# Performance work log

Hardware: AMD Instinct MI355X
Metric: run time of the kernel (lower is better)

## Reference

```python
import jax, jax.numpy as jnp
import numpy as np

B, N, D = 4, 2048, 512
H, DA, DL = 8, 64, 64  # heads, attention_dim, linear_dim
EPS = 1e-6


def _layer_norm(x, eps=EPS):
    # F.layer_norm with no affine params
    mu = jnp.mean(x, axis=-1, keepdims=True)
    var = jnp.var(x, axis=-1, keepdims=True)
    return (x - mu) * jax.lax.rsqrt(var + eps)


def setup_inputs() -> dict:
    key = jax.random.key(0)
    k1, k2, k3, k4 = jax.random.split(key, 4)
    x = jax.random.normal(k1, (B, N, D), dtype=jnp.float32)
    # causal (lower-triangular) valid-attention mask, float {0,1}, shape (B,1,N,N)
    attention_mask = jnp.broadcast_to(
        jnp.tril(jnp.ones((N, N), dtype=jnp.float32))[None, None], (B, 1, N, N)
    )
    # _uvqk: (D, 2*H*DL + 2*H*DA), init normal(0, 0.02)
    uvqk = 0.02 * jax.random.normal(k2, (D, 2 * H * DL + 2 * H * DA), dtype=jnp.float32)
    # _o: Linear(H*DL -> D), xavier uniform
    fan_in, fan_out = H * DL, D
    limit = float(np.sqrt(6.0 / (fan_in + fan_out)))
    o_weight = jax.random.uniform(k3, (fan_out, fan_in), dtype=jnp.float32, minval=-limit, maxval=limit)
    o_bias = jnp.zeros((D,), dtype=jnp.float32)
    return {"x": x, "attention_mask": attention_mask, "uvqk": uvqk,
            "o_weight": o_weight, "o_bias": o_bias}


def reference(x, attention_mask, uvqk, o_weight, o_bias):
    b, n, _ = x.shape
    normed_x = _layer_norm(x)
    mm = jax.nn.silu(normed_x @ uvqk)  # fused uvqk projection + silu
    u, v, q, k = jnp.split(mm, [H * DL, 2 * H * DL, 2 * H * DL + H * DA], axis=-1)
    qh = q.reshape(b, n, H, DA)
    kh = k.reshape(b, n, H, DA)
    vh = v.reshape(b, n, H, DL)
    # silu-activated (non-softmax) attention with mask
    qk = jnp.einsum('bnhd,bmhd->bhnm', qh, kh)
    qk = jax.nn.silu(qk) / n
    qk = qk * attention_mask  # (B,1,N,N) broadcast over heads
    attn = jnp.einsum('bhnm,bmhd->bnhd', qk, vh).reshape(b, n, H * DL)
    # gated norm + output proj + residual
    o_input = u * _layer_norm(attn)
    return o_input @ o_weight.T + o_bias + x
```

## Files before the change

kernel.cpp:

```cpp
#include <hip/hip_runtime.h>

typedef __bf16 bf16x8 __attribute__((ext_vector_type(8)));
typedef float f32x4 __attribute__((ext_vector_type(4)));
typedef float f32x16 __attribute__((ext_vector_type(16)));

__device__ __forceinline__ unsigned short f2bf(float f) {
  return __builtin_bit_cast(unsigned short, (__bf16)f);
}
__device__ __forceinline__ float bfu2f(unsigned short b) {
  unsigned int u = ((unsigned int)b) << 16;
  return __builtin_bit_cast(float, u);
}
__device__ __forceinline__ float silu_f(float x) {
  return x * __builtin_amdgcn_rcpf(1.0f + __expf(-x));
}
__device__ __forceinline__ unsigned pk2(float a, float b) {
  return (unsigned)f2bf(a) | ((unsigned)f2bf(b) << 16);
}

template<int CPR, int NI, bool SWZ = false>
__device__ __forceinline__ void stage16(const __bf16* __restrict__ g, int ld,
                                        __bf16* lds, int wave, int lane) {
#pragma unroll
  for (int t = 0; t < NI; ++t) {
    int cb = (wave * NI + t) * 64;
    int c = cb + lane;
    int row = c / CPR;
    int colb = c % CPR;
    if (SWZ) colb ^= (row & 3);
    __builtin_amdgcn_global_load_lds(
        (const __attribute__((address_space(1))) unsigned int*)(g + row * ld + colb * 8),
        (__attribute__((address_space(3))) unsigned int*)(lds + cb * 8),
        16, 0, 0);
  }
}


__global__ void k_tr_uvqk(const float* __restrict__ uvqk, __bf16* __restrict__ uvqkT) {
  __shared__ float tile[32][33];
  int n0 = blockIdx.x * 32, k0 = blockIdx.y * 32;
  int tx = threadIdx.x, ty = threadIdx.y;
  for (int i = ty; i < 32; i += 8)
    tile[i][tx] = uvqk[(k0 + i) * 2048 + n0 + tx];
  __syncthreads();
  for (int i = ty; i < 32; i += 8)
    uvqkT[(n0 + i) * 512 + k0 + tx] = (__bf16)tile[tx][i];
}

__global__ void k_prep(const float* __restrict__ x, __bf16* __restrict__ nx,
                       const float* __restrict__ ow, __bf16* __restrict__ owb) {
  int bid = blockIdx.x, t = threadIdx.x;
  if (bid >= 8192) {
    int i = (bid - 8192) * 128 + t;
    float4 v = ((const float4*)ow)[i];
    ushort4 o4;
    o4.x = f2bf(v.x); o4.y = f2bf(v.y); o4.z = f2bf(v.z); o4.w = f2bf(v.w);
    ((ushort4*)owb)[i] = o4;
    return;
  }
  float4 v = ((const float4*)(x + (size_t)bid * 512))[t];
  float s = v.x + v.y + v.z + v.w;
  float ss = v.x * v.x + v.y * v.y + v.z * v.z + v.w * v.w;
#pragma unroll
  for (int o = 32; o > 0; o >>= 1) { s += __shfl_down(s, o); ss += __shfl_down(ss, o); }
  __shared__ float red[4];
  if ((t & 63) == 0) { red[(t >> 6) * 2] = s; red[(t >> 6) * 2 + 1] = ss; }
  __syncthreads();
  s = red[0] + red[2]; ss = red[1] + red[3];
  float mu = s * (1.0f / 512.0f);
  float var = ss * (1.0f / 512.0f) - mu * mu;
  float rs = rsqrtf(var + 1e-6f);
  ushort4 o4;
  o4.x = f2bf((v.x - mu) * rs); o4.y = f2bf((v.y - mu) * rs);
  o4.z = f2bf((v.z - mu) * rs); o4.w = f2bf((v.w - mu) * rs);
  ((ushort4*)(nx + (size_t)bid * 512))[t] = o4;
}

__global__ __launch_bounds__(256, 2) void k_proj(
    const __bf16* __restrict__ A, const __bf16* __restrict__ Bt,
    __bf16* __restrict__ u, __bf16* __restrict__ qn,
    __bf16* __restrict__ kn, __bf16* __restrict__ vt) {
  __shared__ __bf16 As[128 * 32], Bs[128 * 32];
  int tid = threadIdx.x, wave = tid >> 6, lane = tid & 63;
  int lr = lane & 15, lq = lane >> 4;
  int bn = blockIdx.x, bm = blockIdx.y;
  const __bf16* Ag = A + (size_t)bm * 128 * 512;
  const __bf16* Bg = Bt + (size_t)bn * 128 * 512;
  int wm = (wave >> 1) * 64, wn = (wave & 1) * 64;
  f32x4 acc[4][4] = {};
  for (int k0 = 0; k0 < 512; k0 += 32) {
    stage16<4, 2>(Ag + k0, 512, As, wave, lane);
    stage16<4, 2>(Bg + k0, 512, Bs, wave, lane);
    __syncthreads();
    bf16x8 a[4], bb[4];
#pragma unroll
    for (int i = 0; i < 4; ++i)
      a[i] = *(const bf16x8*)(As + (wm + i * 16 + lr) * 32 + lq * 8);
#pragma unroll
    for (int j = 0; j < 4; ++j)
      bb[j] = *(const bf16x8*)(Bs + (wn + j * 16 + lr) * 32 + lq * 8);
#pragma unroll
    for (int i = 0; i < 4; ++i)
#pragma unroll
      for (int j = 0; j < 4; ++j)
        acc[i][j] = __builtin_amdgcn_mfma_f32_16x16x32_bf16(a[i], bb[j], acc[i][j], 0, 0, 0);
    __syncthreads();
  }
  int seg = bn >> 2;
  int cb = (bn & 3) * 128 + wn;
  int rb0 = bm * 128 + wm + lq * 4;
  if (seg == 1) {
    const float sc = 1.0f / 2048.0f;
#pragma unroll
    for (int i = 0; i < 4; ++i) {
      int rb = rb0 + i * 16;
      int b = rb >> 11, n = rb & 2047;
#pragma unroll
      for (int j = 0; j < 4; ++j) {
        int c = cb + j * 16 + lr;
        ushort4 w;
        w.x = f2bf(silu_f(acc[i][j][0]) * sc);
        w.y = f2bf(silu_f(acc[i][j][1]) * sc);
        w.z = f2bf(silu_f(acc[i][j][2]) * sc);
        w.w = f2bf(silu_f(acc[i][j][3]) * sc);
        *(ushort4*)(vt + ((size_t)(b * 512 + c)) * 2048 + n) = w;
      }
    }
  } else {
    __bf16* dst = (seg == 0) ? u : ((seg == 2) ? qn : kn);
#pragma unroll
    for (int i = 0; i < 4; ++i) {
      int rb = rb0 + i * 16;
#pragma unroll
      for (int j = 0; j < 4; ++j) {
        int c = cb + j * 16 + lr;
#pragma unroll
        for (int rg = 0; rg < 4; ++rg)
          dst[(size_t)(rb + rg) * 512 + c] = (__bf16)silu_f(acc[i][j][rg]);
      }
    }
  }
}

__global__ __launch_bounds__(256, 2) void k_attn(
    const __bf16* __restrict__ qn, const __bf16* __restrict__ kn,
    const __bf16* __restrict__ vt, __bf16* __restrict__ attn) {
  __shared__ __bf16 lds[40960];
  __bf16* Qs = lds;
  __bf16* Ks0 = lds + 8192;
  __bf16* Ks1 = lds + 16384;
  __bf16* Vs0 = lds + 24576;
  __bf16* Vs1 = lds + 32768;

  int bh = blockIdx.x;
  int yy = blockIdx.y;
  int qt = (yy < 8) ? yy : 23 - yy;
  int b = bh >> 3, h = bh & 7;
  int tid = threadIdx.x, wave = tid >> 6, lane = tid & 63;
  int l31 = lane & 31, lh = lane >> 5;
  int n0 = qt * 128;
  const __bf16* Qg = qn + (size_t)(b * 2048 + n0) * 512 + h * 64;
  const __bf16* Kg = kn + (size_t)(b * 2048) * 512 + h * 64;
  const __bf16* Vg = vt + (size_t)(b * 512 + h * 64) * 2048;

  stage16<4, 2, true>(Qg, 512, Qs, wave, lane);
  stage16<4, 2, true>(Qg + 32, 512, Qs + 4096, wave, lane);
  stage16<4, 2, true>(Kg, 512, Ks0, wave, lane);
  stage16<4, 2, true>(Kg + 32, 512, Ks0 + 4096, wave, lane);
#pragma unroll
  for (int p = 0; p < 4; ++p)
    stage16<4, 1, true>(Vg + p * 32, 2048, Vs0 + p * 2048, wave, lane);
  __syncthreads();

  int wm = (wave >> 1) * 64, wn = (wave & 1) * 64;

  bf16x8 qf[2][4];
#pragma unroll
  for (int j = 0; j < 2; ++j)
#pragma unroll
    for (int ks = 0; ks < 4; ++ks) {
      int row = wn + j * 32 + l31;
      int kidx = ks * 16 + lh * 8;
      qf[j][ks] = *(const bf16x8*)(Qs + (kidx >> 5) * 4096 + row * 32 +
                                   (((kidx & 31)) ^ ((row & 3) * 8)));
    }

  f32x16 po[2][2] = {};

  for (int mt = 0; mt <= qt; ++mt) {
    const __bf16* Kc = (mt & 1) ? Ks1 : Ks0;
    const __bf16* Vc = (mt & 1) ? Vs1 : Vs0;
    if (mt < qt) {
      __bf16* Kn_ = (mt & 1) ? Ks0 : Ks1;
      __bf16* Vn_ = (mt & 1) ? Vs0 : Vs1;
      const __bf16* Kgm = Kg + (size_t)(mt + 1) * 128 * 512;
      stage16<4, 2, true>(Kgm, 512, Kn_, wave, lane);
      stage16<4, 2, true>(Kgm + 32, 512, Kn_ + 4096, wave, lane);
#pragma unroll
      for (int p = 0; p < 4; ++p)
        stage16<4, 1, true>(Vg + (mt + 1) * 128 + p * 32, 2048, Vn_ + p * 2048, wave, lane);
    }
    f32x16 s[2][2] = {};
#pragma unroll
    for (int ks = 0; ks < 4; ++ks) {
      int kidx = ks * 16 + lh * 8;
      bf16x8 ak[2];
#pragma unroll
      for (int i = 0; i < 2; ++i) {
        int row = wm + i * 32 + l31;
        ak[i] = *(const bf16x8*)(Kc + (kidx >> 5) * 4096 + row * 32 +
                                 ((kidx & 31) ^ ((row & 3) * 8)));
      }
#pragma unroll
      for (int i = 0; i < 2; ++i)
#pragma unroll
        for (int j = 0; j < 2; ++j)
          s[i][j] = __builtin_amdgcn_mfma_f32_32x32x16_bf16(ak[i], qf[j][ks], s[i][j], 0, 0, 0);
    }
    bool diag = (mt == qt);
    bool lo = (lh == 0);
    bf16x8 pf[2][4];
#pragma unroll
    for (int i = 0; i < 2; ++i) {
      int mbase = wm + i * 32;
#pragma unroll
      for (int j = 0; j < 2; ++j) {
        int nbase = wn + j * 32;
        bool full = diag && (mbase > nbase + 31);
        unsigned pk[8];
        if (full) {
#pragma unroll
          for (int q = 0; q < 8; ++q) pk[q] = 0u;
        } else {
          bool dtile = diag && (mbase + 31 > nbase);
          int mb = mbase + 4 * lh;
          int ncol = nbase + l31;
          float vv[16];
#pragma unroll
          for (int r = 0; r < 16; ++r) {
            float xx = s[i][j][r];
            float p = xx * __builtin_amdgcn_rcpf(1.0f + __expf(-xx));
            if (dtile) {
              int row = mb + (r & 3) + 8 * (r >> 2);
              if (row > ncol) p = 0.0f;
            }
            vv[r] = p;
          }
#pragma unroll
          for (int q = 0; q < 8; ++q) pk[q] = pk2(vv[2 * q], vv[2 * q + 1]);
        }
        unsigned xa = __shfl_xor(lo ? pk[2] : pk[0], 32);
        unsigned xb = __shfl_xor(lo ? pk[3] : pk[1], 32);
        unsigned xc = __shfl_xor(lo ? pk[6] : pk[4], 32);
        unsigned xd = __shfl_xor(lo ? pk[7] : pk[5], 32);
        union { bf16x8 v; unsigned u[4]; } f0, f1;
        f0.u[0] = lo ? pk[0] : xa;  f0.u[1] = lo ? pk[1] : xb;
        f0.u[2] = lo ? xa : pk[2];  f0.u[3] = lo ? xb : pk[3];
        f1.u[0] = lo ? pk[4] : xc;  f1.u[1] = lo ? pk[5] : xd;
        f1.u[2] = lo ? xc : pk[6];  f1.u[3] = lo ? xd : pk[7];
        pf[j][i * 2 + 0] = f0.v;
        pf[j][i * 2 + 1] = f1.v;
      }
    }
#pragma unroll
    for (int t4 = 0; t4 < 4; ++t4) {
      int kidx = wm + t4 * 16 + lh * 8;
      bf16x8 av[2];
#pragma unroll
      for (int idl = 0; idl < 2; ++idl) {
        int row = idl * 32 + l31;
        av[idl] = *(const bf16x8*)(Vc + (kidx >> 5) * 2048 + row * 32 +
                                   ((kidx & 31) ^ ((row & 3) * 8)));
      }
#pragma unroll
      for (int idl = 0; idl < 2; ++idl)
#pragma unroll
        for (int j = 0; j < 2; ++j)
          po[idl][j] = __builtin_amdgcn_mfma_f32_32x32x16_bf16(av[idl], pf[j][t4], po[idl][j], 0, 0, 0);
    }
    __syncthreads();
  }

  float* red = (float*)lds;
  if (wave >= 2) {
    float* dst = red + (wave - 2) * 4096;
#pragma unroll
    for (int idl = 0; idl < 2; ++idl)
#pragma unroll
      for (int j = 0; j < 2; ++j)
#pragma unroll
        for (int r = 0; r < 16; ++r)
          dst[((idl * 2 + j) * 16 + r) * 64 + lane] = po[idl][j][r];
  }
  __syncthreads();
  __bf16* bo = lds + 24576;
  if (wave < 2) {
    float* src = red + wave * 4096;
#pragma unroll
    for (int idl = 0; idl < 2; ++idl)
#pragma unroll
      for (int j = 0; j < 2; ++j) {
#pragma unroll
        for (int r = 0; r < 16; ++r)
          po[idl][j][r] += src[((idl * 2 + j) * 16 + r) * 64 + lane];
        int nrow = wn + j * 32 + l31;
#pragma unroll
        for (int g = 0; g < 4; ++g) {
          int dl0 = idl * 32 + g * 8 + lh * 4;
          ushort4 w;
          w.x = f2bf(po[idl][j][4 * g + 0]); w.y = f2bf(po[idl][j][4 * g + 1]);
          w.z = f2bf(po[idl][j][4 * g + 2]); w.w = f2bf(po[idl][j][4 * g + 3]);
          *(ushort4*)(bo + nrow * 72 + dl0) = w;
        }
      }
  }
  __syncthreads();
  {
    int n = tid >> 1, part = tid & 1;
    __bf16* gdst = attn + (size_t)(b * 2048 + n0 + n) * 512 + h * 64 + part * 32;
    const __bf16* lsrc = bo + n * 72 + part * 32;
#pragma unroll
    for (int c = 0; c < 4; ++c)
      *(uint4*)(gdst + c * 8) = *(const uint4*)(lsrc + c * 8);
  }
}

__global__ void k_oinput(const __bf16* __restrict__ attn, const __bf16* __restrict__ u,
                         __bf16* __restrict__ oin) {
  int r = blockIdx.x, t = threadIdx.x;
  ushort4 a4 = ((const ushort4*)(attn + (size_t)r * 512))[t];
  float a0 = bfu2f(a4.x), a1 = bfu2f(a4.y), a2 = bfu2f(a4.z), a3 = bfu2f(a4.w);
  float s = a0 + a1 + a2 + a3;
  float ss = a0 * a0 + a1 * a1 + a2 * a2 + a3 * a3;
#pragma unroll
  for (int o = 32; o > 0; o >>= 1) { s += __shfl_down(s, o); ss += __shfl_down(ss, o); }
  __shared__ float red[4];
  if ((t & 63) == 0) { red[(t >> 6) * 2] = s; red[(t >> 6) * 2 + 1] = ss; }
  __syncthreads();
  s = red[0] + red[2]; ss = red[1] + red[3];
  float mu = s * (1.0f / 512.0f);
  float var = ss * (1.0f / 512.0f) - mu * mu;
  float rs = rsqrtf(var + 1e-6f);
  ushort4 u4 = ((const ushort4*)(u + (size_t)r * 512))[t];
  ushort4 o4;
  o4.x = f2bf(bfu2f(u4.x) * (a0 - mu) * rs);
  o4.y = f2bf(bfu2f(u4.y) * (a1 - mu) * rs);
  o4.z = f2bf(bfu2f(u4.z) * (a2 - mu) * rs);
  o4.w = f2bf(bfu2f(u4.w) * (a3 - mu) * rs);
  ((ushort4*)(oin + (size_t)r * 512))[t] = o4;
}

__global__ __launch_bounds__(256, 2) void k_out(
    const __bf16* __restrict__ A, const __bf16* __restrict__ Bt,
    const float* __restrict__ bias, const float* __restrict__ x,
    float* __restrict__ out) {
  __shared__ __bf16 As[128 * 32], Bs[128 * 32];
  int tid = threadIdx.x, wave = tid >> 6, lane = tid & 63;
  int lr = lane & 15, lq = lane >> 4;
  int bn = blockIdx.x, bm = blockIdx.y;
  const __bf16* Ag = A + (size_t)bm * 128 * 512;
  const __bf16* Bg = Bt + (size_t)bn * 128 * 512;
  int wm = (wave >> 1) * 64, wn = (wave & 1) * 64;
  f32x4 acc[4][4] = {};
  for (int k0 = 0; k0 < 512; k0 += 32) {
    stage16<4, 2>(Ag + k0, 512, As, wave, lane);
    stage16<4, 2>(Bg + k0, 512, Bs, wave, lane);
    __syncthreads();
    bf16x8 a[4], bb[4];
#pragma unroll
    for (int i = 0; i < 4; ++i)
      a[i] = *(const bf16x8*)(As + (wm + i * 16 + lr) * 32 + lq * 8);
#pragma unroll
    for (int j = 0; j < 4; ++j)
      bb[j] = *(const bf16x8*)(Bs + (wn + j * 16 + lr) * 32 + lq * 8);
#pragma unroll
    for (int i = 0; i < 4; ++i)
#pragma unroll
      for (int j = 0; j < 4; ++j)
        acc[i][j] = __builtin_amdgcn_mfma_f32_16x16x32_bf16(a[i], bb[j], acc[i][j], 0, 0, 0);
    __syncthreads();
  }
  int cb = bn * 128 + wn;
  int rb0 = bm * 128 + wm + lq * 4;
#pragma unroll
  for (int j = 0; j < 4; ++j) {
    int c = cb + j * 16 + lr;
    float bv = bias[c];
#pragma unroll
    for (int i = 0; i < 4; ++i) {
      int rb = rb0 + i * 16;
#pragma unroll
      for (int rg = 0; rg < 4; ++rg) {
        size_t idx = (size_t)(rb + rg) * 512 + c;
        out[idx] = acc[i][j][rg] + bv + x[idx];
      }
    }
  }
}

extern "C" void kernel_launch(void* const* d_in, const int* in_sizes, int n_in,
                              void* d_out, int out_size, void* d_ws, size_t ws_size,
                              hipStream_t stream) {
  const float* x = (const float*)d_in[0];
  const float* uvqk = (const float*)d_in[2];
  const float* ow = (const float*)d_in[3];
  const float* ob = (const float*)d_in[4];
  float* out = (float*)d_out;

  char* w = (char*)d_ws;
  const size_t MB8 = 8u * 1024 * 1024;
  __bf16* nx    = (__bf16*)(w);
  __bf16* u     = (__bf16*)(w + MB8);
  __bf16* qn    = (__bf16*)(w + 2 * MB8);
  __bf16* kn    = (__bf16*)(w + 3 * MB8);
  __bf16* vt    = (__bf16*)(w + 4 * MB8);
  __bf16* uvqkT = (__bf16*)(w + 5 * MB8);
  __bf16* owb   = (__bf16*)(w + 5 * MB8 + 2097152);
  __bf16* attn  = nx;
  __bf16* o_in  = qn;

  k_tr_uvqk<<<dim3(64, 16), dim3(32, 8), 0, stream>>>(uvqk, uvqkT);
  k_prep<<<8704, 128, 0, stream>>>(x, nx, ow, owb);
  k_proj<<<dim3(16, 64), 256, 0, stream>>>(nx, uvqkT, u, qn, kn, vt);
  k_attn<<<dim3(32, 16), 256, 0, stream>>>(qn, kn, vt, attn);
  k_oinput<<<8192, 128, 0, stream>>>(attn, u, o_in);
  k_out<<<dim3(4, 64), 256, 0, stream>>>(o_in, owb, ob, x, out);
}
```

Baseline: 223.2 us.

## Pair causal query tiles per attention block, halve query tile, widen GEMM K-step

The attention kernel now has each block handle 64 query rows and process two paired query tiles (p and 15-p) in sequence, which evens out causal work per block. The grid becomes 32x8x2. K and V tiles are staged with a single XOR-swizzled 64- or 128-wide layout instead of split 32-wide sub-tiles. The projection and output GEMMs now stage 64-wide K slices with an XOR swizzle, halving the barrier count, and their launch bounds are raised to 3 blocks per CU. The cost is that every attention block re-streams K/V for both query tiles, and per-block MFMA work is smaller.

```diff
diff --git a/kernel.cpp b/kernel.cpp
--- a/kernel.cpp
+++ b/kernel.cpp
@@ -18,7 +18,7 @@
   return (unsigned)f2bf(a) | ((unsigned)f2bf(b) << 16);
 }
 
-template<int CPR, int NI, bool SWZ = false>
+template<int CPR, int NI, int SWZ>
 __device__ __forceinline__ void stage16(const __bf16* __restrict__ g, int ld,
                                         __bf16* lds, int wave, int lane) {
 #pragma unroll
@@ -26,8 +26,7 @@
     int cb = (wave * NI + t) * 64;
     int c = cb + lane;
     int row = c / CPR;
-    int colb = c % CPR;
-    if (SWZ) colb ^= (row & 3);
+    int colb = (c % CPR) ^ (row & SWZ);
     __builtin_amdgcn_global_load_lds(
         (const __attribute__((address_space(1))) unsigned int*)(g + row * ld + colb * 8),
         (__attribute__((address_space(3))) unsigned int*)(lds + cb * 8),
@@ -76,11 +75,11 @@
   ((ushort4*)(nx + (size_t)bid * 512))[t] = o4;
 }
 
-__global__ __launch_bounds__(256, 2) void k_proj(
+__global__ __launch_bounds__(256, 3) void k_proj(
     const __bf16* __restrict__ A, const __bf16* __restrict__ Bt,
     __bf16* __restrict__ u, __bf16* __restrict__ qn,
     __bf16* __restrict__ kn, __bf16* __restrict__ vt) {
-  __shared__ __bf16 As[128 * 32], Bs[128 * 32];
+  __shared__ __bf16 As[128 * 64], Bs[128 * 64];
   int tid = threadIdx.x, wave = tid >> 6, lane = tid & 63;
   int lr = lane & 15, lq = lane >> 4;
   int bn = blockIdx.x, bm = blockIdx.y;
@@ -88,29 +87,36 @@
   const __bf16* Bg = Bt + (size_t)bn * 128 * 512;
   int wm = (wave >> 1) * 64, wn = (wave & 1) * 64;
   f32x4 acc[4][4] = {};
-  for (int k0 = 0; k0 < 512; k0 += 32) {
-    stage16<4, 2>(Ag + k0, 512, As, wave, lane);
-    stage16<4, 2>(Bg + k0, 512, Bs, wave, lane);
-    __syncthreads();
-    bf16x8 a[4], bb[4];
-#pragma unroll
-    for (int i = 0; i < 4; ++i)
-      a[i] = *(const bf16x8*)(As + (wm + i * 16 + lr) * 32 + lq * 8);
-#pragma unroll
-    for (int j = 0; j < 4; ++j)
-      bb[j] = *(const bf16x8*)(Bs + (wn + j * 16 + lr) * 32 + lq * 8);
-#pragma unroll
-    for (int i = 0; i < 4; ++i)
-#pragma unroll
-      for (int j = 0; j < 4; ++j)
-        acc[i][j] = __builtin_amdgcn_mfma_f32_16x16x32_bf16(a[i], bb[j], acc[i][j], 0, 0, 0);
+  for (int k0 = 0; k0 < 512; k0 += 64) {
+    stage16<8, 4, 7>(Ag + k0, 512, As, wave, lane);
+    stage16<8, 4, 7>(Bg + k0, 512, Bs, wave, lane);
+    __syncthreads();
+#pragma unroll
+    for (int kk = 0; kk < 2; ++kk) {
+      int b = kk * 4 + lq;
+      bf16x8 a[4], bb[4];
+#pragma unroll
+      for (int i = 0; i < 4; ++i) {
+        int row = wm + i * 16 + lr;
+        a[i] = *(const bf16x8*)(As + row * 64 + ((b ^ (row & 7)) * 8));
+      }
+#pragma unroll
+      for (int j = 0; j < 4; ++j) {
+        int row = wn + j * 16 + lr;
+        bb[j] = *(const bf16x8*)(Bs + row * 64 + ((b ^ (row & 7)) * 8));
+      }
+#pragma unroll
+      for (int i = 0; i < 4; ++i)
+#pragma unroll
+        for (int j = 0; j < 4; ++j)
+          acc[i][j] = __builtin_amdgcn_mfma_f32_16x16x32_bf16(a[i], bb[j], acc[i][j], 0, 0, 0);
+    }
     __syncthreads();
   }
   int seg = bn >> 2;
   int cb = (bn & 3) * 128 + wn;
   int rb0 = bm * 128 + wm + lq * 4;
   if (seg == 1) {
-    const float sc = 1.0f / 2048.0f;
 #pragma unroll
     for (int i = 0; i < 4; ++i) {
       int rb = rb0 + i * 16;
@@ -119,10 +125,10 @@
       for (int j = 0; j < 4; ++j) {
         int c = cb + j * 16 + lr;
         ushort4 w;
-        w.x = f2bf(silu_f(acc[i][j][0]) * sc);
-        w.y = f2bf(silu_f(acc[i][j][1]) * sc);
-        w.z = f2bf(silu_f(acc[i][j][2]) * sc);
-        w.w = f2bf(silu_f(acc[i][j][3]) * sc);
+        w.x = f2bf(silu_f(acc[i][j][0]) * (1.0f / 2048.0f));
+        w.y = f2bf(silu_f(acc[i][j][1]) * (1.0f / 2048.0f));
+        w.z = f2bf(silu_f(acc[i][j][2]) * (1.0f / 2048.0f));
+        w.w = f2bf(silu_f(acc[i][j][3]) * (1.0f / 2048.0f));
         *(ushort4*)(vt + ((size_t)(b * 512 + c)) * 2048 + n) = w;
       }
     }
@@ -145,106 +151,92 @@
 __global__ __launch_bounds__(256, 2) void k_attn(
     const __bf16* __restrict__ qn, const __bf16* __restrict__ kn,
     const __bf16* __restrict__ vt, __bf16* __restrict__ attn) {
-  __shared__ __bf16 lds[40960];
-  __bf16* Qs = lds;
-  __bf16* Ks0 = lds + 8192;
-  __bf16* Ks1 = lds + 16384;
-  __bf16* Vs0 = lds + 24576;
-  __bf16* Vs1 = lds + 32768;
+  __shared__ __bf16 lds[36864];
+  __bf16* Qs  = lds;
+  __bf16* Ks0 = lds + 4096;
+  __bf16* Ks1 = lds + 12288;
+  __bf16* Vs0 = lds + 20480;
+  __bf16* Vs1 = lds + 28672;
 
   int bh = blockIdx.x;
-  int yy = blockIdx.y;
-  int qt = (yy < 8) ? yy : 23 - yy;
-  int b = bh >> 3, h = bh & 7;
+  int p = blockIdx.y;
+  int half = blockIdx.z;
+  int b = bh >> 3, hd = bh & 7;
   int tid = threadIdx.x, wave = tid >> 6, lane = tid & 63;
   int l31 = lane & 31, lh = lane >> 5;
-  int n0 = qt * 128;
-  const __bf16* Qg = qn + (size_t)(b * 2048 + n0) * 512 + h * 64;
-  const __bf16* Kg = kn + (size_t)(b * 2048) * 512 + h * 64;
-  const __bf16* Vg = vt + (size_t)(b * 512 + h * 64) * 2048;
-
-  stage16<4, 2, true>(Qg, 512, Qs, wave, lane);
-  stage16<4, 2, true>(Qg + 32, 512, Qs + 4096, wave, lane);
-  stage16<4, 2, true>(Kg, 512, Ks0, wave, lane);
-  stage16<4, 2, true>(Kg + 32, 512, Ks0 + 4096, wave, lane);
-#pragma unroll
-  for (int p = 0; p < 4; ++p)
-    stage16<4, 1, true>(Vg + p * 32, 2048, Vs0 + p * 2048, wave, lane);
-  __syncthreads();
-
-  int wm = (wave >> 1) * 64, wn = (wave & 1) * 64;
-
-  bf16x8 qf[2][4];
-#pragma unroll
-  for (int j = 0; j < 2; ++j)
+  int wm = (wave >> 1) * 64, wn = (wave & 1) * 32;
+  const __bf16* Kg = kn + (size_t)(b * 2048) * 512 + hd * 64;
+  const __bf16* Vg = vt + (size_t)(b * 512 + hd * 64) * 2048;
+
+  for (int ph = 0; ph < 2; ++ph) {
+    int qtx = ph ? (15 - p) : p;
+    int n0 = qtx * 128;
+    const __bf16* Qg = qn + (size_t)(b * 2048 + n0 + half * 64) * 512 + hd * 64;
+    if (ph) __syncthreads();
+    stage16<8, 2, 7>(Qg, 512, Qs, wave, lane);
+    stage16<8, 4, 7>(Kg, 512, Ks0, wave, lane);
+    stage16<16, 4, 15>(Vg, 2048, Vs0, wave, lane);
+    __syncthreads();
+
+    bf16x8 qf[4];
 #pragma unroll
     for (int ks = 0; ks < 4; ++ks) {
-      int row = wn + j * 32 + l31;
-      int kidx = ks * 16 + lh * 8;
-      qf[j][ks] = *(const bf16x8*)(Qs + (kidx >> 5) * 4096 + row * 32 +
-                                   (((kidx & 31)) ^ ((row & 3) * 8)));
-    }
-
-  f32x16 po[2][2] = {};
-
-  for (int mt = 0; mt <= qt; ++mt) {
-    const __bf16* Kc = (mt & 1) ? Ks1 : Ks0;
-    const __bf16* Vc = (mt & 1) ? Vs1 : Vs0;
-    if (mt < qt) {
-      __bf16* Kn_ = (mt & 1) ? Ks0 : Ks1;
-      __bf16* Vn_ = (mt & 1) ? Vs0 : Vs1;
-      const __bf16* Kgm = Kg + (size_t)(mt + 1) * 128 * 512;
-      stage16<4, 2, true>(Kgm, 512, Kn_, wave, lane);
-      stage16<4, 2, true>(Kgm + 32, 512, Kn_ + 4096, wave, lane);
-#pragma unroll
-      for (int p = 0; p < 4; ++p)
-        stage16<4, 1, true>(Vg + (mt + 1) * 128 + p * 32, 2048, Vn_ + p * 2048, wave, lane);
-    }
-    f32x16 s[2][2] = {};
-#pragma unroll
-    for (int ks = 0; ks < 4; ++ks) {
-      int kidx = ks * 16 + lh * 8;
-      bf16x8 ak[2];
+      int bk = (ks * 16 + lh * 8) >> 3;
+      int row = wn + l31;
+      qf[ks] = *(const bf16x8*)(Qs + row * 64 + ((bk ^ (row & 7)) * 8));
+    }
+
+    f32x16 po[2] = {};
+
+    for (int mt = 0; mt <= qtx; ++mt) {
+      const __bf16* Kc = (mt & 1) ? Ks1 : Ks0;
+      const __bf16* Vc = (mt & 1) ? Vs1 : Vs0;
+      if (mt < qtx) {
+        __bf16* Kn_ = (mt & 1) ? Ks0 : Ks1;
+        __bf16* Vn_ = (mt & 1) ? Vs0 : Vs1;
+        stage16<8, 4, 7>(Kg + (size_t)(mt + 1) * 128 * 512, 512, Kn_, wave, lane);
+        stage16<16, 4, 15>(Vg + (mt + 1) * 128, 2048, Vn_, wave, lane);
+      }
+      f32x16 s[2] = {};
+#pragma unroll
+      for (int ks = 0; ks < 4; ++ks) {
+        int bk = (ks * 16 + lh * 8) >> 3;
+        bf16x8 ak[2];
+#pragma unroll
+        for (int i = 0; i < 2; ++i) {
+          int row = wm + i * 32 + l31;
+          ak[i] = *(const bf16x8*)(Kc + row * 64 + ((bk ^ (row & 7)) * 8));
+        }
+#pragma unroll
+        for (int i = 0; i < 2; ++i)
+          s[i] = __builtin_amdgcn_mfma_f32_32x32x16_bf16(ak[i], qf[ks], s[i], 0, 0, 0);
+      }
+      bool diag = (mt == qtx);
+      bool lo = (lh == 0);
+      int nb = half * 64 + wn;
+      bf16x8 pf[4];
 #pragma unroll
       for (int i = 0; i < 2; ++i) {
-        int row = wm + i * 32 + l31;
-        ak[i] = *(const bf16x8*)(Kc + (kidx >> 5) * 4096 + row * 32 +
-                                 ((kidx & 31) ^ ((row & 3) * 8)));
-      }
-#pragma unroll
-      for (int i = 0; i < 2; ++i)
-#pragma unroll
-        for (int j = 0; j < 2; ++j)
-          s[i][j] = __builtin_amdgcn_mfma_f32_32x32x16_bf16(ak[i], qf[j][ks], s[i][j], 0, 0, 0);
-    }
-    bool diag = (mt == qt);
-    bool lo = (lh == 0);
-    bf16x8 pf[2][4];
-#pragma unroll
-    for (int i = 0; i < 2; ++i) {
-      int mbase = wm + i * 32;
-#pragma unroll
-      for (int j = 0; j < 2; ++j) {
-        int nbase = wn + j * 32;
-        bool full = diag && (mbase > nbase + 31);
+        int mbase = wm + i * 32;
+        bool full = diag && (mbase > nb + 31);
         unsigned pk[8];
         if (full) {
 #pragma unroll
           for (int q = 0; q < 8; ++q) pk[q] = 0u;
         } else {
-          bool dtile = diag && (mbase + 31 > nbase);
+          bool dtile = diag && (mbase + 31 > nb);
           int mb = mbase + 4 * lh;
-          int ncol = nbase + l31;
+          int ncol = nb + l31;
           float vv[16];
 #pragma unroll
           for (int r = 0; r < 16; ++r) {
-            float xx = s[i][j][r];
-            float p = xx * __builtin_amdgcn_rcpf(1.0f + __expf(-xx));
+            float xx = s[i][r];
+            float pv = xx * __builtin_amdgcn_rcpf(1.0f + __expf(-xx));
             if (dtile) {
               int row = mb + (r & 3) + 8 * (r >> 2);
-              if (row > ncol) p = 0.0f;
+              if (row > ncol) pv = 0.0f;
             }
-            vv[r] = p;
+            vv[r] = pv;
           }
 #pragma unroll
           for (int q = 0; q < 8; ++q) pk[q] = pk2(vv[2 * q], vv[2 * q + 1]);
@@ -258,70 +250,62 @@
         f0.u[2] = lo ? xa : pk[2];  f0.u[3] = lo ? xb : pk[3];
         f1.u[0] = lo ? pk[4] : xc;  f1.u[1] = lo ? pk[5] : xd;
         f1.u[2] = lo ? xc : pk[6];  f1.u[3] = lo ? xd : pk[7];
-        pf[j][i * 2 + 0] = f0.v;
-        pf[j][i * 2 + 1] = f1.v;
-      }
-    }
-#pragma unroll
-    for (int t4 = 0; t4 < 4; ++t4) {
-      int kidx = wm + t4 * 16 + lh * 8;
-      bf16x8 av[2];
+        pf[i * 2 + 0] = f0.v;
+        pf[i * 2 + 1] = f1.v;
+      }
+#pragma unroll
+      for (int t4 = 0; t4 < 4; ++t4) {
+        int bk = (wm + t4 * 16 + lh * 8) >> 3;
+        bf16x8 av[2];
+#pragma unroll
+        for (int idl = 0; idl < 2; ++idl) {
+          int row = idl * 32 + l31;
+          av[idl] = *(const bf16x8*)(Vc + row * 128 + ((bk ^ (row & 15)) * 8));
+        }
+#pragma unroll
+        for (int idl = 0; idl < 2; ++idl)
+          po[idl] = __builtin_amdgcn_mfma_f32_32x32x16_bf16(av[idl], pf[t4], po[idl], 0, 0, 0);
+      }
+      __syncthreads();
+    }
+
+    float* red = (float*)lds;
+    __bf16* bo = lds + 8192;
+    if (wave >= 2) {
+      float* dst = red + (wave - 2) * 2048;
+#pragma unroll
+      for (int idl = 0; idl < 2; ++idl)
+#pragma unroll
+        for (int r = 0; r < 16; ++r)
+          dst[(idl * 16 + r) * 64 + lane] = po[idl][r];
+    }
+    __syncthreads();
+    if (wave < 2) {
+      float* src = red + wave * 2048;
 #pragma unroll
       for (int idl = 0; idl < 2; ++idl) {
-        int row = idl * 32 + l31;
-        av[idl] = *(const bf16x8*)(Vc + (kidx >> 5) * 2048 + row * 32 +
-                                   ((kidx & 31) ^ ((row & 3) * 8)));
-      }
-#pragma unroll
-      for (int idl = 0; idl < 2; ++idl)
-#pragma unroll
-        for (int j = 0; j < 2; ++j)
-          po[idl][j] = __builtin_amdgcn_mfma_f32_32x32x16_bf16(av[idl], pf[j][t4], po[idl][j], 0, 0, 0);
-    }
-    __syncthreads();
-  }
-
-  float* red = (float*)lds;
-  if (wave >= 2) {
-    float* dst = red + (wave - 2) * 4096;
-#pragma unroll
-    for (int idl = 0; idl < 2; ++idl)
-#pragma unroll
-      for (int j = 0; j < 2; ++j)
 #pragma unroll
         for (int r = 0; r < 16; ++r)
-          dst[((idl * 2 + j) * 16 + r) * 64 + lane] = po[idl][j][r];
-  }
-  __syncthreads();
-  __bf16* bo = lds + 24576;
-  if (wave < 2) {
-    float* src = red + wave * 4096;
-#pragma unroll
-    for (int idl = 0; idl < 2; ++idl)
-#pragma unroll
-      for (int j = 0; j < 2; ++j) {
-#pragma unroll
-        for (int r = 0; r < 16; ++r)
-          po[idl][j][r] += src[((idl * 2 + j) * 16 + r) * 64 + lane];
-        int nrow = wn + j * 32 + l31;
+          po[idl][r] += src[(idl * 16 + r) * 64 + lane];
+        int nrow = wn + l31;
 #pragma unroll
         for (int g = 0; g < 4; ++g) {
           int dl0 = idl * 32 + g * 8 + lh * 4;
           ushort4 w;
-          w.x = f2bf(po[idl][j][4 * g + 0]); w.y = f2bf(po[idl][j][4 * g + 1]);
-          w.z = f2bf(po[idl][j][4 * g + 2]); w.w = f2bf(po[idl][j][4 * g + 3]);
+          w.x = f2bf(po[idl][4 * g + 0]); w.y = f2bf(po[idl][4 * g + 1]);
+          w.z = f2bf(po[idl][4 * g + 2]); w.w = f2bf(po[idl][4 * g + 3]);
           *(ushort4*)(bo + nrow * 72 + dl0) = w;
         }
       }
-  }
-  __syncthreads();
-  {
-    int n = tid >> 1, part = tid & 1;
-    __bf16* gdst = attn + (size_t)(b * 2048 + n0 + n) * 512 + h * 64 + part * 32;
-    const __bf16* lsrc = bo + n * 72 + part * 32;
-#pragma unroll
-    for (int c = 0; c < 4; ++c)
-      *(uint4*)(gdst + c * 8) = *(const uint4*)(lsrc + c * 8);
+    }
+    __syncthreads();
+    {
+      int n = tid >> 2, c0 = (tid & 3) * 16;
+      __bf16* gdst = attn + (size_t)(b * 2048 + n0 + half * 64 + n) * 512 + hd * 64 + c0;
+      const __bf16* lsrc = bo + n * 72 + c0;
+      *(uint4*)(gdst) = *(const uint4*)(lsrc);
+      *(uint4*)(gdst + 8) = *(const uint4*)(lsrc + 8);
+    }
   }
 }
 
@@ -350,11 +334,11 @@
   ((ushort4*)(oin + (size_t)r * 512))[t] = o4;
 }
 
-__global__ __launch_bounds__(256, 2) void k_out(
+__global__ __launch_bounds__(256, 3) void k_out(
     const __bf16* __restrict__ A, const __bf16* __restrict__ Bt,
     const float* __restrict__ bias, const float* __restrict__ x,
     float* __restrict__ out) {
-  __shared__ __bf16 As[128 * 32], Bs[128 * 32];
+  __shared__ __bf16 As[128 * 64], Bs[128 * 64];
   int tid = threadIdx.x, wave = tid >> 6, lane = tid & 63;
   int lr = lane & 15, lq = lane >> 4;
   int bn = blockIdx.x, bm = blockIdx.y;
@@ -362,22 +346,30 @@
   const __bf16* Bg = Bt + (size_t)bn * 128 * 512;
   int wm = (wave >> 1) * 64, wn = (wave & 1) * 64;
   f32x4 acc[4][4] = {};
-  for (int k0 = 0; k0 < 512; k0 += 32) {
-    stage16<4, 2>(Ag + k0, 512, As, wave, lane);
-    stage16<4, 2>(Bg + k0, 512, Bs, wave, lane);
-    __syncthreads();
-    bf16x8 a[4], bb[4];
-#pragma unroll
-    for (int i = 0; i < 4; ++i)
-      a[i] = *(const bf16x8*)(As + (wm + i * 16 + lr) * 32 + lq * 8);
-#pragma unroll
-    for (int j = 0; j < 4; ++j)
-      bb[j] = *(const bf16x8*)(Bs + (wn + j * 16 + lr) * 32 + lq * 8);
-#pragma unroll
-    for (int i = 0; i < 4; ++i)
-#pragma unroll
-      for (int j = 0; j < 4; ++j)
-        acc[i][j] = __builtin_amdgcn_mfma_f32_16x16x32_bf16(a[i], bb[j], acc[i][j], 0, 0, 0);
+  for (int k0 = 0; k0 < 512; k0 += 64) {
+    stage16<8, 4, 7>(Ag + k0, 512, As, wave, lane);
+    stage16<8, 4, 7>(Bg + k0, 512, Bs, wave, lane);
+    __syncthreads();
+#pragma unroll
+    for (int kk = 0; kk < 2; ++kk) {
+      int b = kk * 4 + lq;
+      bf16x8 a[4], bb[4];
+#pragma unroll
+      for (int i = 0; i < 4; ++i) {
+        int row = wm + i * 16 + lr;
+        a[i] = *(const bf16x8*)(As + row * 64 + ((b ^ (row & 7)) * 8));
+      }
+#pragma unroll
+      for (int j = 0; j < 4; ++j) {
+        int row = wn + j * 16 + lr;
+        bb[j] = *(const bf16x8*)(Bs + row * 64 + ((b ^ (row & 7)) * 8));
+      }
+#pragma unroll
+      for (int i = 0; i < 4; ++i)
+#pragma unroll
+        for (int j = 0; j < 4; ++j)
+          acc[i][j] = __builtin_amdgcn_mfma_f32_16x16x32_bf16(a[i], bb[j], acc[i][j], 0, 0, 0);
+    }
     __syncthreads();
   }
   int cb = bn * 128 + wn;
@@ -422,7 +414,7 @@
   k_tr_uvqk<<<dim3(64, 16), dim3(32, 8), 0, stream>>>(uvqk, uvqkT);
   k_prep<<<8704, 128, 0, stream>>>(x, nx, ow, owb);
   k_proj<<<dim3(16, 64), 256, 0, stream>>>(nx, uvqkT, u, qn, kn, vt);
-  k_attn<<<dim3(32, 16), 256, 0, stream>>>(qn, kn, vt, attn);
+  k_attn<<<dim3(32, 8, 2), 256, 0, stream>>>(qn, kn, vt, attn);
   k_oinput<<<8192, 128, 0, stream>>>(attn, u, o_in);
   k_out<<<dim3(4, 64), 256, 0, stream>>>(o_in, owb, ob, x, out);
 }
```

Result: faster. 202.9 us (-9.1%).
